# Performance work log

Measured on AMD Instinct MI355X. Metric: run time of the kernel, lower is better.

## Reference

```python
import jax, jax.numpy as jnp
import numpy as np

N, E, IN, HID, Z, H = 10000, 320000, 128, 128, 64, 4


def setup_inputs() -> dict:
    key = jax.random.key(0)
    ks = jax.random.split(key, 24)
    s = 0.05
    inp = {
        "x": jax.random.normal(ks[0], (N, IN), jnp.float32),
        "edge_index": jax.random.randint(ks[1], (2, E), 0, N, jnp.int32),
        "eps": jax.random.normal(ks[2], (N, Z), jnp.float32),
        # GCNConv params
        "gcn_w": jax.random.normal(ks[3], (IN, HID), jnp.float32) * s,
        "gcn_b": jnp.zeros((HID,), jnp.float32),
        # GATConv params (heads=H, out=HID per head, concat=False)
        "gat_w": jax.random.normal(ks[4], (HID, H * HID), jnp.float32) * s,
        "gat_att_src": jax.random.normal(ks[5], (H, HID), jnp.float32) * s,
        "gat_att_dst": jax.random.normal(ks[6], (H, HID), jnp.float32) * s,
        "gat_b": jnp.zeros((HID,), jnp.float32),
        # encoder MLP
        "mlp_w1": jax.random.normal(ks[7], (HID, HID), jnp.float32) * s,
        "mlp_b1": jnp.zeros((HID,), jnp.float32),
        "mlp_w2": jax.random.normal(ks[8], (HID, HID), jnp.float32) * s,
        "mlp_b2": jnp.zeros((HID,), jnp.float32),
        "mu_w": jax.random.normal(ks[9], (HID, Z), jnp.float32) * s,
        "mu_b": jnp.zeros((Z,), jnp.float32),
        "lv_w": jax.random.normal(ks[10], (HID, Z), jnp.float32) * s,
        "lv_b": jnp.zeros((Z,), jnp.float32),
        # decoder
        "dec_w1": jax.random.normal(ks[11], (Z, HID), jnp.float32) * s,
        "dec_b1": jnp.zeros((HID,), jnp.float32),
        "dec_w2": jax.random.normal(ks[12], (HID, Z), jnp.float32) * s,
        "dec_b2": jnp.zeros((Z,), jnp.float32),
    }
    return inp


def _forward(x, eps, gcn_w, gcn_b, gat_w, gat_att_src, gat_att_dst, gat_b,
             mlp_w1, mlp_b1, mlp_w2, mlp_b2, mu_w, mu_b, lv_w, lv_b,
             dec_w1, dec_b1, dec_w2, dec_b2, src, dst):
    n = x.shape[0]
    # ---- GCNConv (symmetric norm, self loops already in src/dst) ----
    h = x @ gcn_w  # [N, HID]
    deg = jax.ops.segment_sum(jnp.ones_like(dst, jnp.float32), dst, num_segments=n)
    dinv = jnp.where(deg > 0, deg ** -0.5, 0.0)
    msg = h[src] * (dinv[src] * dinv[dst])[:, None]  # [E', HID]
    h = jax.nn.relu(jax.ops.segment_sum(msg, dst, num_segments=n) + gcn_b)
    # ---- GATConv (heads=H, concat=False -> mean over heads) ----
    g = (h @ gat_w).reshape(n, H, HID)  # [N,H,D]
    a_src = jnp.einsum("nhd,hd->nh", g, gat_att_src)  # [N,H]
    a_dst = jnp.einsum("nhd,hd->nh", g, gat_att_dst)
    e = jax.nn.leaky_relu(a_src[src] + a_dst[dst], 0.2)  # [E',H]
    emax = jax.ops.segment_max(e, dst, num_segments=n)
    ex = jnp.exp(e - emax[dst])
    den = jax.ops.segment_sum(ex, dst, num_segments=n)
    alpha = ex / den[dst]  # softmax over incoming edges
    agg = jax.ops.segment_sum(alpha[:, :, None] * g[src], dst, num_segments=n)
    h = jax.nn.relu(agg.mean(axis=1) + gat_b)  # [N,HID]
    # ---- MLP ----
    h = jax.nn.relu(h @ mlp_w1 + mlp_b1)
    h = jax.nn.relu(h @ mlp_w2 + mlp_b2)
    mu = h @ mu_w + mu_b
    logvar = h @ lv_w + lv_b
    # ---- reparameterize ----
    lv = jnp.clip(logvar, -10.0, 10.0)
    z = mu + eps * jnp.exp(0.5 * lv)
    # ---- decoder ----
    d = jax.nn.relu(z @ dec_w1 + dec_b1)
    d = d @ dec_w2 + dec_b2 + z
    logits = d @ d.T  # [N,N]
    return logits, mu, logvar


def reference(x, edge_index, eps, gcn_w, gcn_b, gat_w, gat_att_src, gat_att_dst,
              gat_b, mlp_w1, mlp_b1, mlp_w2, mlp_b2, mu_w, mu_b, lv_w, lv_b,
              dec_w1, dec_b1, dec_w2, dec_b2):
    n = x.shape[0]
    loop = jnp.arange(n, dtype=edge_index.dtype)
    src = jnp.concatenate([edge_index[0], loop])
    dst = jnp.concatenate([edge_index[1], loop])
    return _forward(x, eps, gcn_w, gcn_b, gat_w, gat_att_src, gat_att_dst,
                    gat_b, mlp_w1, mlp_b1, mlp_w2, mlp_b2, mu_w, mu_b,
                    lv_w, lv_b, dec_w1, dec_b1, dec_w2, dec_b2, src, dst)
```

## Files before the change

### kernel.cpp

```cpp
#include <hip/hip_runtime.h>
#include <hip/hip_bf16.h>

typedef unsigned short u16;
typedef unsigned int u32;

#define NN 10000
#define EE 320000

typedef __attribute__((ext_vector_type(8))) short short8;
typedef __attribute__((ext_vector_type(4))) float f32x4;

__device__ __forceinline__ u16 f2bfu(float f) {
    u32 x = __float_as_uint(f);
    x += 0x7FFFu + ((x >> 16) & 1u);
    return (u16)(x >> 16);
}
__device__ __forceinline__ void ld4f(const float* p, float* o) {
    float4 v = *(const float4*)p; o[0] = v.x; o[1] = v.y; o[2] = v.z; o[3] = v.w;
}

__global__ void k_hist(const int* __restrict__ dst, int* __restrict__ cnt) {
    int e = blockIdx.x * 256 + threadIdx.x;
    if (e < EE) atomicAdd(&cnt[dst[e]], 1);
}

__global__ void k_dinv(const int* __restrict__ cnt, float* __restrict__ dinv) {
    int n = blockIdx.x * 256 + threadIdx.x;
    if (n < NN) dinv[n] = 1.f / sqrtf((float)(cnt[n] + 1));
}

__global__ void k_scan(const int* __restrict__ cnt, int* __restrict__ rowptr) {
    __shared__ int sh[1024];
    int t = threadIdx.x;
    int base = t * 10;
    int loc[10];
    int s = 0;
    #pragma unroll
    for (int i = 0; i < 10; i++) {
        int idx = base + i;
        int v = (idx < NN) ? cnt[idx] : 0;
        loc[i] = s; s += v;
    }
    sh[t] = s;
    __syncthreads();
    for (int off = 1; off < 1024; off <<= 1) {
        int v = (t >= off) ? sh[t - off] : 0;
        __syncthreads();
        sh[t] += v;
        __syncthreads();
    }
    int ex = sh[t] - s;
    #pragma unroll
    for (int i = 0; i < 10; i++) {
        int idx = base + i;
        if (idx < NN) rowptr[idx] = ex + loc[i];
    }
    if (t == 0) rowptr[NN] = EE;
}

__global__ void k_scatter(const int* __restrict__ src, const int* __restrict__ dst,
                          const int* __restrict__ rowptr, int* __restrict__ fill,
                          int* __restrict__ csr) {
    int e = blockIdx.x * 256 + threadIdx.x;
    if (e < EE) {
        int d = dst[e];
        int pos = rowptr[d] + atomicAdd(&fill[d], 1);
        csr[pos] = src[e];
    }
}

template <int K, int M, bool RELU, bool BIAS>
__global__ __launch_bounds__(256) void k_linear(const float* __restrict__ A, const float* __restrict__ W,
                                                const float* __restrict__ Bb, float* __restrict__ out) {
    constexpr int MC = M / 64;
    int wid = (blockIdx.x * blockDim.x + threadIdx.x) >> 6;
    int lane = threadIdx.x & 63;
    int row0 = wid * 4;
    if (row0 >= NN) return;
    float acc[4][MC];
    #pragma unroll
    for (int i = 0; i < 4; i++)
        #pragma unroll
        for (int j = 0; j < MC; j++) acc[i][j] = 0.f;
    for (int k = 0; k < K; k += 4) {
        float a[4][4];
        #pragma unroll
        for (int i = 0; i < 4; i++) ld4f(A + (size_t)(row0 + i) * K + k, a[i]);
        #pragma unroll
        for (int kk = 0; kk < 4; kk++) {
            float wv[MC];
            #pragma unroll
            for (int j = 0; j < MC; j++) wv[j] = W[(size_t)(k + kk) * M + j * 64 + lane];
            #pragma unroll
            for (int i = 0; i < 4; i++)
                #pragma unroll
                for (int j = 0; j < MC; j++) acc[i][j] += a[i][kk] * wv[j];
        }
    }
    #pragma unroll
    for (int i = 0; i < 4; i++) {
        int r = row0 + i;
        #pragma unroll
        for (int j = 0; j < MC; j++) {
            float v = acc[i][j];
            if constexpr (BIAS) v += Bb[j * 64 + lane];
            if constexpr (RELU) v = fmaxf(v, 0.f);
            out[(size_t)r * M + j * 64 + lane] = v;
        }
    }
}

__global__ __launch_bounds__(256) void k_gcn_agg(const float* __restrict__ h0, const int* __restrict__ rowptr,
                                                 const int* __restrict__ csr, const float* __restrict__ dinv,
                                                 const float* __restrict__ bias, float* __restrict__ h1) {
    int node = (blockIdx.x * blockDim.x + threadIdx.x) >> 6;
    int lane = threadIdx.x & 63;
    if (node >= NN) return;
    float di = dinv[node];
    const float* hn = h0 + (size_t)node * 128;
    float acc0 = hn[lane] * di * di;
    float acc1 = hn[64 + lane] * di * di;
    int st = rowptr[node], en = rowptr[node + 1];
    for (int p = st; p < en; p++) {
        int s = csr[p];
        float w = dinv[s] * di;
        const float* hs = h0 + (size_t)s * 128;
        acc0 += hs[lane] * w;
        acc1 += hs[64 + lane] * w;
    }
    acc0 += bias[lane];
    acc1 += bias[64 + lane];
    h1[(size_t)node * 128 + lane] = fmaxf(acc0, 0.f);
    h1[(size_t)node * 128 + 64 + lane] = fmaxf(acc1, 0.f);
}

__global__ __launch_bounds__(256) void k_gat_scores(const float* __restrict__ g, const float* __restrict__ att_s,
                                                    const float* __restrict__ att_d, float* __restrict__ a_src,
                                                    float* __restrict__ a_dst) {
    int node = (blockIdx.x * blockDim.x + threadIdx.x) >> 6;
    int lane = threadIdx.x & 63;
    if (node >= NN) return;
    const float* gp = g + (size_t)node * 512 + lane * 8;
    float gv[8];
    ld4f(gp, gv); ld4f(gp + 4, gv + 4);
    float sv[8], dv[8];
    ld4f(att_s + lane * 8, sv); ld4f(att_s + lane * 8 + 4, sv + 4);
    ld4f(att_d + lane * 8, dv); ld4f(att_d + lane * 8 + 4, dv + 4);
    float ps = 0.f, pd = 0.f;
    #pragma unroll
    for (int i = 0; i < 8; i++) { ps += gv[i] * sv[i]; pd += gv[i] * dv[i]; }
    for (int off = 1; off < 16; off <<= 1) {
        ps += __shfl_xor(ps, off, 64);
        pd += __shfl_xor(pd, off, 64);
    }
    if ((lane & 15) == 0) {
        int h = lane >> 4;
        a_src[node * 4 + h] = ps;
        a_dst[node * 4 + h] = pd;
    }
}

__global__ __launch_bounds__(256) void k_gat_softmax(const int* __restrict__ rowptr, const int* __restrict__ csr,
                                                     const float* __restrict__ a_src, const float* __restrict__ a_dst,
                                                     float* __restrict__ alpha, float* __restrict__ selfalpha) {
    int node = (blockIdx.x * blockDim.x + threadIdx.x) >> 6;
    int lane = threadIdx.x & 63;
    if (node >= NN) return;
    float ad[4], asn[4];
    ld4f(a_dst + node * 4, ad);
    ld4f(a_src + node * 4, asn);
    float es[4], m[4];
    #pragma unroll
    for (int h = 0; h < 4; h++) {
        float e = asn[h] + ad[h];
        es[h] = e > 0.f ? e : 0.2f * e;
        m[h] = es[h];
    }
    int st = rowptr[node], en = rowptr[node + 1];
    for (int p = st + lane; p < en; p += 64) {
        int s = csr[p];
        float as[4]; ld4f(a_src + s * 4, as);
        #pragma unroll
        for (int h = 0; h < 4; h++) {
            float e = as[h] + ad[h];
            e = e > 0.f ? e : 0.2f * e;
            m[h] = fmaxf(m[h], e);
        }
    }
    #pragma unroll
    for (int h = 0; h < 4; h++)
        for (int off = 1; off < 64; off <<= 1) m[h] = fmaxf(m[h], __shfl_xor(m[h], off, 64));
    float den[4];
    #pragma unroll
    for (int h = 0; h < 4; h++) den[h] = (lane == 0) ? __expf(es[h] - m[h]) : 0.f;
    for (int p = st + lane; p < en; p += 64) {
        int s = csr[p];
        float as[4]; ld4f(a_src + s * 4, as);
        #pragma unroll
        for (int h = 0; h < 4; h++) {
            float e = as[h] + ad[h];
            e = e > 0.f ? e : 0.2f * e;
            den[h] += __expf(e - m[h]);
        }
    }
    #pragma unroll
    for (int h = 0; h < 4; h++)
        for (int off = 1; off < 64; off <<= 1) den[h] += __shfl_xor(den[h], off, 64);
    float inv[4];
    #pragma unroll
    for (int h = 0; h < 4; h++) inv[h] = 1.f / den[h];
    for (int p = st + lane; p < en; p += 64) {
        int s = csr[p];
        float as[4]; ld4f(a_src + s * 4, as);
        float4 al;
        float av[4];
        #pragma unroll
        for (int h = 0; h < 4; h++) {
            float e = as[h] + ad[h];
            e = e > 0.f ? e : 0.2f * e;
            av[h] = __expf(e - m[h]) * inv[h];
        }
        al.x = av[0]; al.y = av[1]; al.z = av[2]; al.w = av[3];
        *(float4*)(alpha + (size_t)p * 4) = al;
    }
    if (lane == 0) {
        float4 sa;
        sa.x = __expf(es[0] - m[0]) * inv[0];
        sa.y = __expf(es[1] - m[1]) * inv[1];
        sa.z = __expf(es[2] - m[2]) * inv[2];
        sa.w = __expf(es[3] - m[3]) * inv[3];
        *(float4*)(selfalpha + (size_t)node * 4) = sa;
    }
}

__global__ __launch_bounds__(256) void k_gat_agg(const float* __restrict__ g, const int* __restrict__ rowptr,
                                                 const int* __restrict__ csr, const float* __restrict__ alpha,
                                                 const float* __restrict__ selfalpha, const float* __restrict__ bias,
                                                 float* __restrict__ h2) {
    int node = (blockIdx.x * blockDim.x + threadIdx.x) >> 6;
    int lane = threadIdx.x & 63;
    if (node >= NN) return;
    float sa[4];
    ld4f(selfalpha + (size_t)node * 4, sa);
    const float* gn = g + (size_t)node * 512;
    float acc0 = 0.f, acc1 = 0.f;
    #pragma unroll
    for (int h = 0; h < 4; h++) {
        acc0 += sa[h] * gn[h * 128 + lane];
        acc1 += sa[h] * gn[h * 128 + 64 + lane];
    }
    int st = rowptr[node], en = rowptr[node + 1];
    for (int p = st; p < en; p++) {
        int s = csr[p];
        float al[4];
        ld4f(alpha + (size_t)p * 4, al);
        const float* gs = g + (size_t)s * 512;
        #pragma unroll
        for (int h = 0; h < 4; h++) {
            acc0 += al[h] * gs[h * 128 + lane];
            acc1 += al[h] * gs[h * 128 + 64 + lane];
        }
    }
    acc0 = fmaxf(acc0 * 0.25f + bias[lane], 0.f);
    acc1 = fmaxf(acc1 * 0.25f + bias[64 + lane], 0.f);
    h2[(size_t)node * 128 + lane] = acc0;
    h2[(size_t)node * 128 + 64 + lane] = acc1;
}

__global__ __launch_bounds__(256) void k_mu(const float* __restrict__ A, const float* __restrict__ W,
                                            const float* __restrict__ Bb, float* __restrict__ mu_out) {
    int wid = (blockIdx.x * blockDim.x + threadIdx.x) >> 6;
    int lane = threadIdx.x & 63;
    int row0 = wid * 4;
    if (row0 >= NN) return;
    float acc[4] = {0.f, 0.f, 0.f, 0.f};
    for (int k = 0; k < 128; k += 4) {
        float a[4][4];
        #pragma unroll
        for (int i = 0; i < 4; i++) ld4f(A + (size_t)(row0 + i) * 128 + k, a[i]);
        #pragma unroll
        for (int kk = 0; kk < 4; kk++) {
            float wv = W[(k + kk) * 64 + lane];
            #pragma unroll
            for (int i = 0; i < 4; i++) acc[i] += a[i][kk] * wv;
        }
    }
    float b = Bb[lane];
    #pragma unroll
    for (int i = 0; i < 4; i++)
        mu_out[(size_t)(row0 + i) * 64 + lane] = acc[i] + b;
}

__global__ __launch_bounds__(256) void k_lv(const float* __restrict__ A, const float* __restrict__ W,
                                            const float* __restrict__ Bb, const float* __restrict__ mu,
                                            const float* __restrict__ eps, float* __restrict__ z,
                                            float* __restrict__ lv_out) {
    int wid = (blockIdx.x * blockDim.x + threadIdx.x) >> 6;
    int lane = threadIdx.x & 63;
    int row0 = wid * 4;
    if (row0 >= NN) return;
    float acc[4] = {0.f, 0.f, 0.f, 0.f};
    for (int k = 0; k < 128; k += 4) {
        float a[4][4];
        #pragma unroll
        for (int i = 0; i < 4; i++) ld4f(A + (size_t)(row0 + i) * 128 + k, a[i]);
        #pragma unroll
        for (int kk = 0; kk < 4; kk++) {
            float wv = W[(k + kk) * 64 + lane];
            #pragma unroll
            for (int i = 0; i < 4; i++) acc[i] += a[i][kk] * wv;
        }
    }
    float b = Bb[lane];
    #pragma unroll
    for (int i = 0; i < 4; i++) {
        size_t idx = (size_t)(row0 + i) * 64 + lane;
        float lv = acc[i] + b;
        lv_out[idx] = lv;
        float c = fminf(fmaxf(lv, -10.f), 10.f);
        z[idx] = mu[idx] + eps[idx] * __expf(0.5f * c);
    }
}

__global__ __launch_bounds__(256) void k_dec2(const float* __restrict__ A, const float* __restrict__ W,
                                              const float* __restrict__ Bb, const float* __restrict__ z,
                                              u16* __restrict__ dbf) {
    int wid = (blockIdx.x * blockDim.x + threadIdx.x) >> 6;
    int lane = threadIdx.x & 63;
    int row0 = wid * 4;
    if (row0 >= NN) return;
    float acc[4] = {0.f, 0.f, 0.f, 0.f};
    for (int k = 0; k < 128; k += 4) {
        float a[4][4];
        #pragma unroll
        for (int i = 0; i < 4; i++) ld4f(A + (size_t)(row0 + i) * 128 + k, a[i]);
        #pragma unroll
        for (int kk = 0; kk < 4; kk++) {
            float wv = W[(k + kk) * 64 + lane];
            #pragma unroll
            for (int i = 0; i < 4; i++) acc[i] += a[i][kk] * wv;
        }
    }
    float b = Bb[lane];
    #pragma unroll
    for (int i = 0; i < 4; i++) {
        size_t idx = (size_t)(row0 + i) * 64 + lane;
        dbf[idx] = f2bfu(acc[i] + b + z[idx]);
    }
}

__global__ __launch_bounds__(256) void k_logits(const u16* __restrict__ dbf, float* __restrict__ out) {
    __shared__ float tile[64][132];
    int tid = threadIdx.x;
    int wave = tid >> 6;
    int lane = tid & 63;
    int l15 = lane & 15, quad = lane >> 4;
    int rowhalf = wave >> 1;
    int i0 = blockIdx.y * 128 + rowhalf * 64;
    int j0 = blockIdx.x * 128 + (wave & 1) * 64;

    f32x4 acc[4][4];
    #pragma unroll
    for (int r = 0; r < 4; r++)
        #pragma unroll
        for (int c = 0; c < 4; c++) acc[r][c] = (f32x4){0.f, 0.f, 0.f, 0.f};

    #pragma unroll
    for (int ks = 0; ks < 64; ks += 32) {
        short8 a[4], b[4];
        #pragma unroll
        for (int r = 0; r < 4; r++) {
            int row = i0 + r * 16 + l15;
            if (row < NN) a[r] = *(const short8*)(dbf + (size_t)row * 64 + ks + quad * 8);
            else a[r] = (short8){0, 0, 0, 0, 0, 0, 0, 0};
        }
        #pragma unroll
        for (int c = 0; c < 4; c++) {
            int row = j0 + c * 16 + l15;
            if (row < NN) b[c] = *(const short8*)(dbf + (size_t)row * 64 + ks + quad * 8);
            else b[c] = (short8){0, 0, 0, 0, 0, 0, 0, 0};
        }
        #pragma unroll
        for (int r = 0; r < 4; r++)
            #pragma unroll
            for (int c = 0; c < 4; c++)
                acc[r][c] = __builtin_amdgcn_mfma_f32_16x16x32_bf16(a[r], b[c], acc[r][c], 0, 0, 0);
    }

    int lc0 = (wave & 1) * 64;
    #pragma unroll
    for (int chunk = 0; chunk < 2; chunk++) {
        if (rowhalf == chunk) {
            #pragma unroll
            for (int r = 0; r < 4; r++)
                #pragma unroll
                for (int c = 0; c < 4; c++)
                    #pragma unroll
                    for (int v = 0; v < 4; v++)
                        tile[r * 16 + quad * 4 + v][lc0 + c * 16 + l15] = acc[r][c][v];
        }
        __syncthreads();
        #pragma unroll
        for (int it = 0; it < 8; it++) {
            int idx = it * 256 + tid;
            int row = idx >> 5, ch = idx & 31;
            int rg = blockIdx.y * 128 + chunk * 64 + row;
            int cg = blockIdx.x * 128 + ch * 4;
            if (rg < NN && cg < NN) {
                float4 v = *(const float4*)&tile[row][ch * 4];
                *(float4*)(out + (size_t)rg * NN + cg) = v;
            }
        }
        __syncthreads();
    }
}

extern "C" void kernel_launch(void* const* d_in, const int* in_sizes, int n_in,
                              void* d_out, int out_size, void* d_ws, size_t ws_size,
                              hipStream_t stream) {
    const float* x      = (const float*)d_in[0];
    const int*   ei     = (const int*)d_in[1];
    const float* eps    = (const float*)d_in[2];
    const float* gcn_w  = (const float*)d_in[3];
    const float* gcn_b  = (const float*)d_in[4];
    const float* gat_w  = (const float*)d_in[5];
    const float* att_s  = (const float*)d_in[6];
    const float* att_d  = (const float*)d_in[7];
    const float* gat_b  = (const float*)d_in[8];
    const float* mlp_w1 = (const float*)d_in[9];
    const float* mlp_b1 = (const float*)d_in[10];
    const float* mlp_w2 = (const float*)d_in[11];
    const float* mlp_b2 = (const float*)d_in[12];
    const float* mu_w   = (const float*)d_in[13];
    const float* mu_b   = (const float*)d_in[14];
    const float* lv_w   = (const float*)d_in[15];
    const float* lv_b   = (const float*)d_in[16];
    const float* dec_w1 = (const float*)d_in[17];
    const float* dec_b1 = (const float*)d_in[18];
    const float* dec_w2 = (const float*)d_in[19];
    const float* dec_b2 = (const float*)d_in[20];

    float* out    = (float*)d_out;
    float* out_mu = out + (size_t)NN * NN;
    float* out_lv = out_mu + (size_t)NN * 64;

    char* ws = (char*)d_ws;
    size_t off = 0;
    auto alloc = [&](size_t bytes) -> void* {
        void* p = ws + off;
        off += (bytes + 255) & ~(size_t)255;
        return p;
    };
    int*   cnt       = (int*)alloc(NN * 4);
    int*   fill      = (int*)alloc(NN * 4);
    int*   rowptr    = (int*)alloc((NN + 1) * 4);
    int*   csr       = (int*)alloc(EE * 4);
    float* dinv      = (float*)alloc(NN * 4);
    float* a_src     = (float*)alloc(NN * 4 * 4);
    float* a_dst     = (float*)alloc(NN * 4 * 4);
    float* selfalpha = (float*)alloc(NN * 4 * 4);
    float* z         = (float*)alloc((size_t)NN * 64 * 4);
    float* h2        = (float*)alloc((size_t)NN * 128 * 4);
    float* bufA      = (float*)alloc((size_t)NN * 128 * 4);
    float* bufB      = (float*)alloc((size_t)NN * 128 * 4);
    float* bufC      = (float*)alloc((size_t)NN * 512 * 4);
    float* bufD      = (float*)alloc((size_t)EE * 4 * 4);

    float* h0    = bufA;
    float* h1    = bufB;
    float* g     = bufC;
    float* alpha = bufD;
    float* m1    = bufA;
    float* m2    = bufB;
    float* t1    = bufC;
    u16*   dbf   = (u16*)bufD;

    const int* src = ei;
    const int* dst = ei + EE;

    hipMemsetAsync(cnt, 0, NN * 4, stream);
    hipMemsetAsync(fill, 0, NN * 4, stream);

    k_hist<<<(EE + 255) / 256, 256, 0, stream>>>(dst, cnt);
    k_dinv<<<(NN + 255) / 256, 256, 0, stream>>>(cnt, dinv);
    k_scan<<<1, 1024, 0, stream>>>(cnt, rowptr);
    k_scatter<<<(EE + 255) / 256, 256, 0, stream>>>(src, dst, rowptr, fill, csr);

    k_linear<128, 128, false, false><<<625, 256, 0, stream>>>(x, gcn_w, nullptr, h0);
    k_gcn_agg<<<2500, 256, 0, stream>>>(h0, rowptr, csr, dinv, gcn_b, h1);

    k_linear<128, 512, false, false><<<625, 256, 0, stream>>>(h1, gat_w, nullptr, g);
    k_gat_scores<<<2500, 256, 0, stream>>>(g, att_s, att_d, a_src, a_dst);
    k_gat_softmax<<<2500, 256, 0, stream>>>(rowptr, csr, a_src, a_dst, alpha, selfalpha);
    k_gat_agg<<<2500, 256, 0, stream>>>(g, rowptr, csr, alpha, selfalpha, gat_b, h2);

    k_linear<128, 128, true, true><<<625, 256, 0, stream>>>(h2, mlp_w1, mlp_b1, m1);
    k_linear<128, 128, true, true><<<625, 256, 0, stream>>>(m1, mlp_w2, mlp_b2, m2);
    k_mu<<<625, 256, 0, stream>>>(m2, mu_w, mu_b, out_mu);
    k_lv<<<625, 256, 0, stream>>>(m2, lv_w, lv_b, out_mu, eps, z, out_lv);

    k_linear<64, 128, true, true><<<625, 256, 0, stream>>>(z, dec_w1, dec_b1, t1);
    k_dec2<<<625, 256, 0, stream>>>(t1, dec_w2, dec_b2, z, dbf);

    dim3 lgrid((NN + 127) / 128, (NN + 127) / 128);
    k_logits<<<lgrid, 256, 0, stream>>>(dbf, out);
}
```

Before: 802.2 us.

## Store GCN/GAT features in bf16, fuse GAT scores and mu/logvar heads, nontemporal logits

The GCN linear output and the GAT projected features are now stored as bf16, which halves the bytes gathered per edge in the two aggregation kernels. The GAT attention scores are computed inside the GAT linear kernel, and the mu and logvar heads are merged into one kernel, so intermediates are no longer re-read from memory. GAT aggregation is reorganised so each lane handles 8 contiguous features of one head and uses a shuffle reduction across heads. The large logits write now uses nontemporal stores to bypass the cache. The cost is some precision loss in the aggregated features from bf16 rounding.

```diff
diff --git a/kernel.cpp b/kernel.cpp
--- a/kernel.cpp
+++ b/kernel.cpp
@@ -15,6 +15,7 @@
     x += 0x7FFFu + ((x >> 16) & 1u);
     return (u16)(x >> 16);
 }
+__device__ __forceinline__ float bfu2f(u16 u) { return __uint_as_float(((u32)u) << 16); }
 __device__ __forceinline__ void ld4f(const float* p, float* o) {
     float4 v = *(const float4*)p; o[0] = v.x; o[1] = v.y; o[2] = v.z; o[3] = v.w;
 }
@@ -69,9 +70,9 @@
     }
 }
 
-template <int K, int M, bool RELU, bool BIAS>
+template <int K, int M, bool RELU, bool BIAS, bool OB16>
 __global__ __launch_bounds__(256) void k_linear(const float* __restrict__ A, const float* __restrict__ W,
-                                                const float* __restrict__ Bb, float* __restrict__ out) {
+                                                const float* __restrict__ Bb, void* __restrict__ outv) {
     constexpr int MC = M / 64;
     int wid = (blockIdx.x * blockDim.x + threadIdx.x) >> 6;
     int lane = threadIdx.x & 63;
@@ -97,6 +98,8 @@
                 for (int j = 0; j < MC; j++) acc[i][j] += a[i][kk] * wv[j];
         }
     }
+    float* outf = (float*)outv;
+    u16*   outb = (u16*)outv;
     #pragma unroll
     for (int i = 0; i < 4; i++) {
         int r = row0 + i;
@@ -105,58 +108,87 @@
             float v = acc[i][j];
             if constexpr (BIAS) v += Bb[j * 64 + lane];
             if constexpr (RELU) v = fmaxf(v, 0.f);
-            out[(size_t)r * M + j * 64 + lane] = v;
-        }
-    }
-}
-
-__global__ __launch_bounds__(256) void k_gcn_agg(const float* __restrict__ h0, const int* __restrict__ rowptr,
+            if constexpr (OB16) outb[(size_t)r * M + j * 64 + lane] = f2bfu(v);
+            else                outf[(size_t)r * M + j * 64 + lane] = v;
+        }
+    }
+}
+
+__global__ __launch_bounds__(256) void k_gcn_agg(const u16* __restrict__ h0, const int* __restrict__ rowptr,
                                                  const int* __restrict__ csr, const float* __restrict__ dinv,
                                                  const float* __restrict__ bias, float* __restrict__ h1) {
     int node = (blockIdx.x * blockDim.x + threadIdx.x) >> 6;
     int lane = threadIdx.x & 63;
     if (node >= NN) return;
     float di = dinv[node];
-    const float* hn = h0 + (size_t)node * 128;
-    float acc0 = hn[lane] * di * di;
-    float acc1 = hn[64 + lane] * di * di;
+    u32 sv = *(const u32*)(h0 + (size_t)node * 128 + lane * 2);
+    float acc0 = bfu2f((u16)(sv & 0xffffu)) * di * di;
+    float acc1 = bfu2f((u16)(sv >> 16)) * di * di;
     int st = rowptr[node], en = rowptr[node + 1];
     for (int p = st; p < en; p++) {
         int s = csr[p];
         float w = dinv[s] * di;
-        const float* hs = h0 + (size_t)s * 128;
-        acc0 += hs[lane] * w;
-        acc1 += hs[64 + lane] * w;
-    }
-    acc0 += bias[lane];
-    acc1 += bias[64 + lane];
-    h1[(size_t)node * 128 + lane] = fmaxf(acc0, 0.f);
-    h1[(size_t)node * 128 + 64 + lane] = fmaxf(acc1, 0.f);
-}
-
-__global__ __launch_bounds__(256) void k_gat_scores(const float* __restrict__ g, const float* __restrict__ att_s,
-                                                    const float* __restrict__ att_d, float* __restrict__ a_src,
+        u32 gv = *(const u32*)(h0 + (size_t)s * 128 + lane * 2);
+        acc0 += bfu2f((u16)(gv & 0xffffu)) * w;
+        acc1 += bfu2f((u16)(gv >> 16)) * w;
+    }
+    acc0 = fmaxf(acc0 + bias[lane * 2], 0.f);
+    acc1 = fmaxf(acc1 + bias[lane * 2 + 1], 0.f);
+    float2 o; o.x = acc0; o.y = acc1;
+    *(float2*)(h1 + (size_t)node * 128 + lane * 2) = o;
+}
+
+__global__ __launch_bounds__(256) void k_gat_linear(const float* __restrict__ A, const float* __restrict__ W,
+                                                    const float* __restrict__ att_s, const float* __restrict__ att_d,
+                                                    u16* __restrict__ gbf, float* __restrict__ a_src,
                                                     float* __restrict__ a_dst) {
-    int node = (blockIdx.x * blockDim.x + threadIdx.x) >> 6;
-    int lane = threadIdx.x & 63;
-    if (node >= NN) return;
-    const float* gp = g + (size_t)node * 512 + lane * 8;
-    float gv[8];
-    ld4f(gp, gv); ld4f(gp + 4, gv + 4);
+    int wid = (blockIdx.x * blockDim.x + threadIdx.x) >> 6;
+    int lane = threadIdx.x & 63;
+    int row0 = wid * 4;
+    if (row0 >= NN) return;
+    float acc[4][8];
+    #pragma unroll
+    for (int i = 0; i < 4; i++)
+        #pragma unroll
+        for (int t = 0; t < 8; t++) acc[i][t] = 0.f;
+    for (int k = 0; k < 128; k += 4) {
+        float a[4][4];
+        #pragma unroll
+        for (int i = 0; i < 4; i++) ld4f(A + (size_t)(row0 + i) * 128 + k, a[i]);
+        #pragma unroll
+        for (int kk = 0; kk < 4; kk++) {
+            float wv[8];
+            ld4f(W + (size_t)(k + kk) * 512 + lane * 8, wv);
+            ld4f(W + (size_t)(k + kk) * 512 + lane * 8 + 4, wv + 4);
+            #pragma unroll
+            for (int i = 0; i < 4; i++)
+                #pragma unroll
+                for (int t = 0; t < 8; t++) acc[i][t] += a[i][kk] * wv[t];
+        }
+    }
     float sv[8], dv[8];
     ld4f(att_s + lane * 8, sv); ld4f(att_s + lane * 8 + 4, sv + 4);
     ld4f(att_d + lane * 8, dv); ld4f(att_d + lane * 8 + 4, dv + 4);
-    float ps = 0.f, pd = 0.f;
-    #pragma unroll
-    for (int i = 0; i < 8; i++) { ps += gv[i] * sv[i]; pd += gv[i] * dv[i]; }
-    for (int off = 1; off < 16; off <<= 1) {
-        ps += __shfl_xor(ps, off, 64);
-        pd += __shfl_xor(pd, off, 64);
-    }
-    if ((lane & 15) == 0) {
-        int h = lane >> 4;
-        a_src[node * 4 + h] = ps;
-        a_dst[node * 4 + h] = pd;
+    int head = lane >> 4;
+    #pragma unroll
+    for (int i = 0; i < 4; i++) {
+        int r = row0 + i;
+        short8 pk;
+        #pragma unroll
+        for (int t = 0; t < 8; t++) pk[t] = (short)f2bfu(acc[i][t]);
+        *(short8*)(gbf + (size_t)r * 512 + lane * 8) = pk;
+        float ps = 0.f, pd = 0.f;
+        #pragma unroll
+        for (int t = 0; t < 8; t++) { ps += acc[i][t] * sv[t]; pd += acc[i][t] * dv[t]; }
+        #pragma unroll
+        for (int off = 1; off < 16; off <<= 1) {
+            ps += __shfl_xor(ps, off, 64);
+            pd += __shfl_xor(pd, off, 64);
+        }
+        if ((lane & 15) == i) {
+            a_src[r * 4 + head] = ps;
+            a_dst[r * 4 + head] = pd;
+        }
     }
 }
 
@@ -233,92 +265,78 @@
     }
 }
 
-__global__ __launch_bounds__(256) void k_gat_agg(const float* __restrict__ g, const int* __restrict__ rowptr,
+__global__ __launch_bounds__(256) void k_gat_agg(const u16* __restrict__ gbf, const int* __restrict__ rowptr,
                                                  const int* __restrict__ csr, const float* __restrict__ alpha,
                                                  const float* __restrict__ selfalpha, const float* __restrict__ bias,
                                                  float* __restrict__ h2) {
     int node = (blockIdx.x * blockDim.x + threadIdx.x) >> 6;
     int lane = threadIdx.x & 63;
     if (node >= NN) return;
-    float sa[4];
-    ld4f(selfalpha + (size_t)node * 4, sa);
-    const float* gn = g + (size_t)node * 512;
-    float acc0 = 0.f, acc1 = 0.f;
-    #pragma unroll
-    for (int h = 0; h < 4; h++) {
-        acc0 += sa[h] * gn[h * 128 + lane];
-        acc1 += sa[h] * gn[h * 128 + 64 + lane];
-    }
+    int head = lane >> 4;
+    float acc[8];
+    float sa = selfalpha[(size_t)node * 4 + head];
+    short8 gs = *(const short8*)(gbf + (size_t)node * 512 + lane * 8);
+    #pragma unroll
+    for (int t = 0; t < 8; t++) acc[t] = sa * bfu2f((u16)gs[t]);
     int st = rowptr[node], en = rowptr[node + 1];
     for (int p = st; p < en; p++) {
         int s = csr[p];
-        float al[4];
-        ld4f(alpha + (size_t)p * 4, al);
-        const float* gs = g + (size_t)s * 512;
-        #pragma unroll
-        for (int h = 0; h < 4; h++) {
-            acc0 += al[h] * gs[h * 128 + lane];
-            acc1 += al[h] * gs[h * 128 + 64 + lane];
-        }
-    }
-    acc0 = fmaxf(acc0 * 0.25f + bias[lane], 0.f);
-    acc1 = fmaxf(acc1 * 0.25f + bias[64 + lane], 0.f);
-    h2[(size_t)node * 128 + lane] = acc0;
-    h2[(size_t)node * 128 + 64 + lane] = acc1;
-}
-
-__global__ __launch_bounds__(256) void k_mu(const float* __restrict__ A, const float* __restrict__ W,
-                                            const float* __restrict__ Bb, float* __restrict__ mu_out) {
+        float al = alpha[(size_t)p * 4 + head];
+        short8 gv = *(const short8*)(gbf + (size_t)s * 512 + lane * 8);
+        #pragma unroll
+        for (int t = 0; t < 8; t++) acc[t] += al * bfu2f((u16)gv[t]);
+    }
+    #pragma unroll
+    for (int t = 0; t < 8; t++) {
+        acc[t] += __shfl_xor(acc[t], 16, 64);
+        acc[t] += __shfl_xor(acc[t], 32, 64);
+    }
+    if (lane < 16) {
+        int d0 = lane * 8;
+        float o[8];
+        #pragma unroll
+        for (int t = 0; t < 8; t++) o[t] = fmaxf(acc[t] * 0.25f + bias[d0 + t], 0.f);
+        float4 v0, v1;
+        v0.x = o[0]; v0.y = o[1]; v0.z = o[2]; v0.w = o[3];
+        v1.x = o[4]; v1.y = o[5]; v1.z = o[6]; v1.w = o[7];
+        *(float4*)(h2 + (size_t)node * 128 + d0) = v0;
+        *(float4*)(h2 + (size_t)node * 128 + d0 + 4) = v1;
+    }
+}
+
+__global__ __launch_bounds__(256) void k_heads(const float* __restrict__ A, const float* __restrict__ muW,
+                                               const float* __restrict__ muB, const float* __restrict__ lvW,
+                                               const float* __restrict__ lvB, const float* __restrict__ eps,
+                                               float* __restrict__ mu_out, float* __restrict__ lv_out,
+                                               float* __restrict__ z) {
     int wid = (blockIdx.x * blockDim.x + threadIdx.x) >> 6;
     int lane = threadIdx.x & 63;
     int row0 = wid * 4;
     if (row0 >= NN) return;
-    float acc[4] = {0.f, 0.f, 0.f, 0.f};
+    float am[4] = {0.f, 0.f, 0.f, 0.f};
+    float av[4] = {0.f, 0.f, 0.f, 0.f};
     for (int k = 0; k < 128; k += 4) {
         float a[4][4];
         #pragma unroll
         for (int i = 0; i < 4; i++) ld4f(A + (size_t)(row0 + i) * 128 + k, a[i]);
         #pragma unroll
         for (int kk = 0; kk < 4; kk++) {
-            float wv = W[(k + kk) * 64 + lane];
-            #pragma unroll
-            for (int i = 0; i < 4; i++) acc[i] += a[i][kk] * wv;
-        }
-    }
-    float b = Bb[lane];
-    #pragma unroll
-    for (int i = 0; i < 4; i++)
-        mu_out[(size_t)(row0 + i) * 64 + lane] = acc[i] + b;
-}
-
-__global__ __launch_bounds__(256) void k_lv(const float* __restrict__ A, const float* __restrict__ W,
-                                            const float* __restrict__ Bb, const float* __restrict__ mu,
-                                            const float* __restrict__ eps, float* __restrict__ z,
-                                            float* __restrict__ lv_out) {
-    int wid = (blockIdx.x * blockDim.x + threadIdx.x) >> 6;
-    int lane = threadIdx.x & 63;
-    int row0 = wid * 4;
-    if (row0 >= NN) return;
-    float acc[4] = {0.f, 0.f, 0.f, 0.f};
-    for (int k = 0; k < 128; k += 4) {
-        float a[4][4];
-        #pragma unroll
-        for (int i = 0; i < 4; i++) ld4f(A + (size_t)(row0 + i) * 128 + k, a[i]);
-        #pragma unroll
-        for (int kk = 0; kk < 4; kk++) {
-            float wv = W[(k + kk) * 64 + lane];
-            #pragma unroll
-            for (int i = 0; i < 4; i++) acc[i] += a[i][kk] * wv;
-        }
-    }
-    float b = Bb[lane];
+            float wm = muW[(k + kk) * 64 + lane];
+            float wl = lvW[(k + kk) * 64 + lane];
+            #pragma unroll
+            for (int i = 0; i < 4; i++) { am[i] += a[i][kk] * wm; av[i] += a[i][kk] * wl; }
+        }
+    }
+    float bm = muB[lane], bl = lvB[lane];
     #pragma unroll
     for (int i = 0; i < 4; i++) {
         size_t idx = (size_t)(row0 + i) * 64 + lane;
-        float lv = acc[i] + b;
+        float mu = am[i] + bm;
+        float lv = av[i] + bl;
+        mu_out[idx] = mu;
         lv_out[idx] = lv;
         float c = fminf(fmaxf(lv, -10.f), 10.f);
-        z[idx] = mu[idx] + eps[idx] * __expf(0.5f * c);
+        z[idx] = mu + eps[idx] * __expf(0.5f * c);
     }
 }
 
@@ -407,8 +425,8 @@
             int rg = blockIdx.y * 128 + chunk * 64 + row;
             int cg = blockIdx.x * 128 + ch * 4;
             if (rg < NN && cg < NN) {
-                float4 v = *(const float4*)&tile[row][ch * 4];
-                *(float4*)(out + (size_t)rg * NN + cg) = v;
+                f32x4 v = *(const f32x4*)&tile[row][ch * 4];
+                __builtin_nontemporal_store(v, (f32x4*)(out + (size_t)rg * NN + cg));
             }
         }
         __syncthreads();
@@ -466,9 +484,9 @@
     float* bufC      = (float*)alloc((size_t)NN * 512 * 4);
     float* bufD      = (float*)alloc((size_t)EE * 4 * 4);
 
-    float* h0    = bufA;
+    u16*   h0bf  = (u16*)bufA;
     float* h1    = bufB;
-    float* g     = bufC;
+    u16*   gbf   = (u16*)bufC;
     float* alpha = bufD;
     float* m1    = bufA;
     float* m2    = bufB;
@@ -486,20 +504,18 @@
     k_scan<<<1, 1024, 0, stream>>>(cnt, rowptr);
     k_scatter<<<(EE + 255) / 256, 256, 0, stream>>>(src, dst, rowptr, fill, csr);
 
-    k_linear<128, 128, false, false><<<625, 256, 0, stream>>>(x, gcn_w, nullptr, h0);
-    k_gcn_agg<<<2500, 256, 0, stream>>>(h0, rowptr, csr, dinv, gcn_b, h1);
-
-    k_linear<128, 512, false, false><<<625, 256, 0, stream>>>(h1, gat_w, nullptr, g);
-    k_gat_scores<<<2500, 256, 0, stream>>>(g, att_s, att_d, a_src, a_dst);
+    k_linear<128, 128, false, false, true><<<625, 256, 0, stream>>>(x, gcn_w, nullptr, h0bf);
+    k_gcn_agg<<<2500, 256, 0, stream>>>(h0bf, rowptr, csr, dinv, gcn_b, h1);
+
+    k_gat_linear<<<625, 256, 0, stream>>>(h1, gat_w, att_s, att_d, gbf, a_src, a_dst);
     k_gat_softmax<<<2500, 256, 0, stream>>>(rowptr, csr, a_src, a_dst, alpha, selfalpha);
-    k_gat_agg<<<2500, 256, 0, stream>>>(g, rowptr, csr, alpha, selfalpha, gat_b, h2);
-
-    k_linear<128, 128, true, true><<<625, 256, 0, stream>>>(h2, mlp_w1, mlp_b1, m1);
-    k_linear<128, 128, true, true><<<625, 256, 0, stream>>>(m1, mlp_w2, mlp_b2, m2);
-    k_mu<<<625, 256, 0, stream>>>(m2, mu_w, mu_b, out_mu);
-    k_lv<<<625, 256, 0, stream>>>(m2, lv_w, lv_b, out_mu, eps, z, out_lv);
-
-    k_linear<64, 128, true, true><<<625, 256, 0, stream>>>(z, dec_w1, dec_b1, t1);
+    k_gat_agg<<<2500, 256, 0, stream>>>(gbf, rowptr, csr, alpha, selfalpha, gat_b, h2);
+
+    k_linear<128, 128, true, true, false><<<625, 256, 0, stream>>>(h2, mlp_w1, mlp_b1, m1);
+    k_linear<128, 128, true, true, false><<<625, 256, 0, stream>>>(m1, mlp_w2, mlp_b2, m2);
+    k_heads<<<625, 256, 0, stream>>>(m2, mu_w, mu_b, lv_w, lv_b, eps, out_mu, out_lv, z);
+
+    k_linear<64, 128, true, true, false><<<625, 256, 0, stream>>>(z, dec_w1, dec_b1, t1);
     k_dec2<<<625, 256, 0, stream>>>(t1, dec_w2, dec_b2, z, dbf);
 
     dim3 lgrid((NN + 127) / 128, (NN + 127) / 128);
```

New measurement: 760.8 us. -5.2%, faster.
